# Kernel tuning notes

Hardware: AMD Instinct MI355X
Metric: run time of the kernel (lower is better)

The kernel has to match this reference:

```python
import jax, jax.numpy as jnp
import numpy as np

B, IN_SHAPE, EXP_SHAPE, HID, NB_CLASSES = 64, 10000, 53, 1500, 2048


def setup_inputs() -> dict:
    key = jax.random.key(0)
    ks = jax.random.split(key, 8)
    gos = jax.random.uniform(ks[0], (B, IN_SHAPE), dtype=jnp.float32)
    exp_x = jax.random.uniform(ks[1], (B, EXP_SHAPE), dtype=jnp.float32)
    # FlatModel params (torch Linear: y = x @ W.T + b; store pre-transposed)
    W1 = jax.random.normal(ks[2], (IN_SHAPE, HID), dtype=jnp.float32) * (1.0 / np.sqrt(IN_SHAPE))
    b1 = jnp.zeros((HID,), dtype=jnp.float32)
    W2 = jax.random.normal(ks[3], (HID + EXP_SHAPE, NB_CLASSES), dtype=jnp.float32) * (1.0 / np.sqrt(HID + EXP_SHAPE))
    b2 = jnp.zeros((NB_CLASSES,), dtype=jnp.float32)
    # HPO adjacency (non-trainable buffer in the original; values in [0,1))
    hpo_matrix = jax.random.uniform(ks[4], (NB_CLASSES, NB_CLASSES), dtype=jnp.float32)
    return {"gos": gos, "exp_x": exp_x, "W1": W1, "b1": b1, "W2": W2, "b2": b2, "hpo_matrix": hpo_matrix}


def reference(gos, exp_x, W1, b1, W2, b2, hpo_matrix):
    # FlatModel (eval mode: dropout is identity). torch F.gelu default = exact erf gelu.
    h = jax.nn.gelu(gos @ W1 + b1, approximate=False)          # (B, HID)
    x = jnp.concatenate([h, exp_x], axis=1)                     # (B, HID+EXP)
    flat = jax.nn.sigmoid(x @ W2 + b2)                          # (B, C)
    # HPOLayer + permute + MaxPool1d(C): out[b,j] = max_i flat[b,j] * M[i,j]
    out = jnp.max(flat[:, None, :] * hpo_matrix[None, :, :], axis=1)  # (B, C)
    return out
```

## Files before the change

### kernel.cpp

```cpp
#include <hip/hip_runtime.h>
#include <math.h>

#define B64 64
#define IN_SH 10000
#define EXP_SH 53
#define HID 1500
#define NPAD1 1536
#define NBC 2048
#define K2 1553
#define KS1 20
#define KST1 16
#define KS2 7
#define KST2 8
#define XSTEP 56
#define CMCH 32
#define CMBLK 256
#define WLDS 640

using short8  = __attribute__((ext_vector_type(8))) short;
using floatx4 = __attribute__((ext_vector_type(4))) float;
using uintx4  = __attribute__((ext_vector_type(4))) unsigned int;

__device__ __forceinline__ unsigned short f2bf(float f) {
    unsigned u = __float_as_uint(f);
    u += 0x7fffu + ((u >> 16) & 1u);
    return (unsigned short)(u >> 16);
}


__global__ __launch_bounds__(256) void prep_k(const float* __restrict__ g,
                                              unsigned short* __restrict__ gosBf,
                                              float* __restrict__ accz) {
    int bi = blockIdx.x;
    if (bi < 320) {
        int t    = bi * 256 + threadIdx.x;
        int lane = t & 63;
        int sgrp = (t >> 6) & 3;
        int step = t >> 8;
        int q    = lane >> 4;
        int l15  = lane & 15;
        int b    = sgrp * 16 + l15;
        int k0   = step * 32 + q * 8;
        const float* p = g + (size_t)b * IN_SH + k0;
        unsigned int o[4];
        #pragma unroll
        for (int i = 0; i < 4; i++) {
            float lo = (k0 + 2 * i     < IN_SH) ? p[2 * i]     : 0.f;
            float hi = (k0 + 2 * i + 1 < IN_SH) ? p[2 * i + 1] : 0.f;
            o[i] = (unsigned)f2bf(lo) | ((unsigned)f2bf(hi) << 16);
        }
        uintx4 v; v.x = o[0]; v.y = o[1]; v.z = o[2]; v.w = o[3];
        *(uintx4*)(gosBf + (size_t)t * 8) = v;
    } else {
        int t = (bi - 320) * 256 + threadIdx.x;
        floatx4 z = (floatx4){0.f, 0.f, 0.f, 0.f};
        #pragma unroll
        for (int i = 0; i < 28; i++)
            *(floatx4*)(accz + (size_t)(i * 2048 + t) * 4) = z;
    }
}

__device__ __forceinline__ void load_b4(const unsigned short* __restrict__ bf,
                                        int stg, uintx4 bv[4]) {
    #pragma unroll
    for (int s = 0; s < 4; s++)
        bv[s] = *(const uintx4*)(bf + (size_t)(stg * 4 + s) * 512);
}

template<int KSTEPS>
__device__ __forceinline__ void gemm_core(
    const float* __restrict__ W, const unsigned short* __restrict__ Bfc,
    float* __restrict__ accbuf, int N, int K, int ldw, int bx, int by, int tid,
    float* __restrict__ ldsw)
{
    int lane = tid & 63;
    int q    = lane >> 4;
    int l15  = lane & 15;
    int n0   = bx * 64 + 16 * (tid >> 6);
    int k0   = by * (KSTEPS * 32);
    bool fast = (n0 + 16 <= N) && (k0 + KSTEPS * 32 <= K);
    int kl  = lane >> 2;
    int c4  = (lane & 3) * 4;

    const unsigned short* bf = Bfc + (size_t)lane * 8;

    floatx4 acc[4];
    #pragma unroll
    for (int s = 0; s < 4; s++) acc[s] = (floatx4){0.f, 0.f, 0.f, 0.f};

    floatx4 g[2][2];

    #define GLB(st, slot)                                                        \
        {                                                                        \
            int kb_ = k0 + (st) * 32;                                            \
            _Pragma("unroll")                                                    \
            for (int i_ = 0; i_ < 2; i_++) {                                     \
                int kg_ = kb_ + kl + 16 * i_;                                    \
                if (fast) {                                                      \
                    g[slot][i_] = *(const floatx4*)(W + (size_t)kg_ * ldw + n0 + c4); \
                } else {                                                         \
                    _Pragma("unroll")                                            \
                    for (int j_ = 0; j_ < 4; j_++)                               \
                        g[slot][i_][j_] = (kg_ < K && n0 + c4 + j_ < N)          \
                            ? W[(size_t)kg_ * ldw + n0 + c4 + j_] : 0.f;         \
                }                                                                \
            }                                                                    \
        }
    #define LWR(buf, slot)                                                       \
        {                                                                        \
            _Pragma("unroll")                                                    \
            for (int i_ = 0; i_ < 2; i_++)                                       \
                *(floatx4*)(ldsw + (buf) * WLDS + (kl + 16 * i_) * 20 + c4) = g[slot][i_]; \
        }

    GLB(0, 0);
    if (KSTEPS > 1) GLB(1, 1);
    LWR(0, 0);

    uintx4 bv[2][4];
    load_b4(bf, 0, bv[0]);
    if (KSTEPS > 1) load_b4(bf, 1, bv[1]);

    #pragma unroll
    for (int st = 0; st < KSTEPS; st++) {
        const int s = st & 1;
        const float* lb = ldsw + s * WLDS;

        short8 af;
        #pragma unroll
        for (int j = 0; j < 8; j++)
            af[j] = (short)f2bf(lb[(q * 8 + j) * 20 + l15]);

        uintx4 bt[4];
        if (st + 2 < KSTEPS) {
            GLB(st + 2, s);
            load_b4(bf, st + 2, bt);
        }

        #pragma unroll
        for (int m = 0; m < 4; m++) {
            short8 bf8 = __builtin_bit_cast(short8, bv[s][m]);
            acc[m] = __builtin_amdgcn_mfma_f32_16x16x32_bf16(af, bf8, acc[m], 0, 0, 0);
        }

        if (st + 1 < KSTEPS) LWR(1 - s, 1 - s);
        if (st + 2 < KSTEPS) {
            #pragma unroll
            for (int m = 0; m < 4; m++) bv[s][m] = bt[m];
        }
    }
    #undef GLB
    #undef LWR

    int nrow = n0 + q * 4;
    #pragma unroll
    for (int s = 0; s < 4; s++) {
        #pragma unroll
        for (int rr = 0; rr < 4; rr++)
            atomicAdd(&accbuf[(size_t)(nrow + rr) * 64 + s * 16 + l15], acc[s][rr]);
    }
}

__global__ __launch_bounds__(256) void gemm1_k(
    const float* __restrict__ W1, const unsigned short* __restrict__ gosBf,
    float* __restrict__ hpre, const float* __restrict__ M, float* __restrict__ cm)
{
    __shared__ float lds[4 * 2 * WLDS];
    int bi = blockIdx.x;
    if (bi < CMBLK) {
        int j  = (bi & 7) * 256 + threadIdx.x;
        int i0 = (bi >> 3) * 64;
        float m = 0.0f;
        #pragma unroll 16
        for (int i = i0; i < i0 + 64; i++)
            m = fmaxf(m, M[(size_t)i * NBC + j]);
        cm[(bi >> 3) * NBC + j] = m;
    } else {
        int gb = bi - CMBLK;
        int bx = gb % 24;
        int by = gb / 24;
        gemm_core<KST1>(W1, gosBf + (size_t)by * (KST1 * 4) * 512,
                        hpre, HID, IN_SH, HID, bx, by,
                        threadIdx.x, lds + (threadIdx.x >> 6) * (2 * WLDS));
    }
}

__global__ __launch_bounds__(256) void gemm2_k(
    const float* __restrict__ W2, const unsigned short* __restrict__ Xf,
    float* __restrict__ logits)
{
    __shared__ float lds[4 * 2 * WLDS];
    gemm_core<KST2>(W2, Xf + (size_t)blockIdx.y * (KST2 * 4) * 512,
                    logits, NBC, K2, NBC, blockIdx.x, blockIdx.y,
                    threadIdx.x, lds + (threadIdx.x >> 6) * (2 * WLDS));
}

__global__ __launch_bounds__(256) void combine1(
    const float* __restrict__ hpre, const float* __restrict__ b1,
    const float* __restrict__ expx, unsigned short* __restrict__ Xf,
    const float* __restrict__ cm, float* __restrict__ cmr)
{
    int bi = blockIdx.x;
    if (bi < XSTEP) {
        int t    = bi * 256 + threadIdx.x;
        int lane = t & 63;
        int sgrp = (t >> 6) & 3;
        int step = t >> 8;
        int q    = lane >> 4;
        int l15  = lane & 15;
        int b    = sgrp * 16 + l15;
        int kb   = step * 32 + q * 8;
        unsigned int o[4];
        #pragma unroll
        for (int i = 0; i < 4; i++) {
            unsigned int lohi[2];
            #pragma unroll
            for (int h = 0; h < 2; h++) {
                int n = kb + 2 * i + h;
                float v = 0.f;
                if (n < HID) {
                    float s = hpre[(size_t)n * 64 + b] + b1[n];
                    v = 0.5f * s * (1.0f + erff(s * 0.70710678118654752f));
                } else if (n < HID + EXP_SH) {
                    v = expx[b * EXP_SH + (n - HID)];
                }
                lohi[h] = f2bf(v);
            }
            o[i] = lohi[0] | (lohi[1] << 16);
        }
        uintx4 v; v.x = o[0]; v.y = o[1]; v.z = o[2]; v.w = o[3];
        *(uintx4*)(Xf + (size_t)t * 8) = v;
    } else {
        int j = (bi - XSTEP) * 256 + threadIdx.x;
        float m = 0.f;
        #pragma unroll
        for (int c = 0; c < CMCH; c++) m = fmaxf(m, cm[c * NBC + j]);
        cmr[j] = m;
    }
}

__global__ __launch_bounds__(256) void final_k(
    const float* __restrict__ logits, const float* __restrict__ b2,
    const float* __restrict__ cmr, float* __restrict__ out)
{
    int idx = blockIdx.x * 256 + threadIdx.x;
    int b = idx & 63;
    int j = idx >> 6;
    float s = logits[(size_t)j * 64 + b] + b2[j];
    float sig = 1.0f / (1.0f + expf(-s));
    out[(size_t)b * NBC + j] = sig * cmr[j];
}

extern "C" void kernel_launch(void* const* d_in, const int* in_sizes, int n_in,
                              void* d_out, int out_size, void* d_ws, size_t ws_size,
                              hipStream_t stream) {
    const float* gos  = (const float*)d_in[0];
    const float* expx = (const float*)d_in[1];
    const float* W1   = (const float*)d_in[2];
    const float* b1   = (const float*)d_in[3];
    const float* W2   = (const float*)d_in[4];
    const float* b2   = (const float*)d_in[5];
    const float* hpo  = (const float*)d_in[6];
    float* out = (float*)d_out;

    char* ws = (char*)d_ws;
    unsigned short* gosBf = (unsigned short*)ws;
    float* hpre   = (float*)(ws + 1310720);
    float* logits = (float*)(ws + 1310720 + 393216);
    unsigned short* Xf = (unsigned short*)(ws + 2228224);
    float* cm  = (float*)(ws + 2228224 + 229376);
    float* cmr = (float*)(ws + 2228224 + 229376 + 262144);

    prep_k<<<328, 256, 0, stream>>>(gos, gosBf, hpre);

    gemm1_k<<<CMBLK + 24 * KS1, 256, 0, stream>>>(W1, gosBf, hpre, hpo, cm);

    combine1<<<XSTEP + 8, 256, 0, stream>>>(hpre, b1, expx, Xf, cm, cmr);

    gemm2_k<<<dim3(NBC / 64, KS2), 256, 0, stream>>>(W2, Xf, logits);

    final_k<<<(B64 * NBC) / 256, 256, 0, stream>>>(logits, b2, cmr, out);
}
```

Measured before the change: 154.0 us.

## Replace atomic split-K accumulation with per-slice partial buffers and doubled K splits

```diff
diff --git a/kernel.cpp b/kernel.cpp
--- a/kernel.cpp
+++ b/kernel.cpp
@@ -1,5 +1,6 @@
 #include <hip/hip_runtime.h>
 #include <math.h>
+
 
 #define B64 64
 #define IN_SH 10000
@@ -8,18 +9,21 @@
 #define NPAD1 1536
 #define NBC 2048
 #define K2 1553
-#define KS1 20
-#define KST1 16
-#define KS2 7
-#define KST2 8
+#define KS1 40
+#define KST1 8
+#define KS2 13
+#define KST2 4
 #define XSTEP 56
 #define CMCH 32
 #define CMBLK 256
 #define WLDS 640
+#define ACC1 (NPAD1 * 64)
+#define ACC2 (NBC * 64)
 
 using short8  = __attribute__((ext_vector_type(8))) short;
 using floatx4 = __attribute__((ext_vector_type(4))) float;
 using uintx4  = __attribute__((ext_vector_type(4))) unsigned int;
+using uintx2  = __attribute__((ext_vector_type(2))) unsigned int;
 
 __device__ __forceinline__ unsigned short f2bf(float f) {
     unsigned u = __float_as_uint(f);
@@ -29,35 +33,25 @@
 
 
 __global__ __launch_bounds__(256) void prep_k(const float* __restrict__ g,
-                                              unsigned short* __restrict__ gosBf,
-                                              float* __restrict__ accz) {
-    int bi = blockIdx.x;
-    if (bi < 320) {
-        int t    = bi * 256 + threadIdx.x;
-        int lane = t & 63;
-        int sgrp = (t >> 6) & 3;
-        int step = t >> 8;
-        int q    = lane >> 4;
-        int l15  = lane & 15;
-        int b    = sgrp * 16 + l15;
-        int k0   = step * 32 + q * 8;
-        const float* p = g + (size_t)b * IN_SH + k0;
-        unsigned int o[4];
-        #pragma unroll
-        for (int i = 0; i < 4; i++) {
-            float lo = (k0 + 2 * i     < IN_SH) ? p[2 * i]     : 0.f;
-            float hi = (k0 + 2 * i + 1 < IN_SH) ? p[2 * i + 1] : 0.f;
-            o[i] = (unsigned)f2bf(lo) | ((unsigned)f2bf(hi) << 16);
-        }
-        uintx4 v; v.x = o[0]; v.y = o[1]; v.z = o[2]; v.w = o[3];
-        *(uintx4*)(gosBf + (size_t)t * 8) = v;
-    } else {
-        int t = (bi - 320) * 256 + threadIdx.x;
-        floatx4 z = (floatx4){0.f, 0.f, 0.f, 0.f};
-        #pragma unroll
-        for (int i = 0; i < 28; i++)
-            *(floatx4*)(accz + (size_t)(i * 2048 + t) * 4) = z;
-    }
+                                              unsigned short* __restrict__ gosBf) {
+    int t    = blockIdx.x * 256 + threadIdx.x;
+    int lane = t & 63;
+    int sgrp = (t >> 6) & 3;
+    int step = t >> 8;
+    int q    = lane >> 4;
+    int l15  = lane & 15;
+    int b    = sgrp * 16 + l15;
+    int k0   = step * 32 + q * 8;
+    const float* p = g + (size_t)b * IN_SH + k0;
+    unsigned int o[4];
+    #pragma unroll
+    for (int i = 0; i < 4; i++) {
+        float lo = (k0 + 2 * i     < IN_SH) ? p[2 * i]     : 0.f;
+        float hi = (k0 + 2 * i + 1 < IN_SH) ? p[2 * i + 1] : 0.f;
+        o[i] = (unsigned)f2bf(lo) | ((unsigned)f2bf(hi) << 16);
+    }
+    uintx4 v; v.x = o[0]; v.y = o[1]; v.z = o[2]; v.w = o[3];
+    *(uintx4*)(gosBf + (size_t)t * 8) = v;
 }
 
 __device__ __forceinline__ void load_b4(const unsigned short* __restrict__ bf,
@@ -70,7 +64,7 @@
 template<int KSTEPS>
 __device__ __forceinline__ void gemm_core(
     const float* __restrict__ W, const unsigned short* __restrict__ Bfc,
-    float* __restrict__ accbuf, int N, int K, int ldw, int bx, int by, int tid,
+    float* __restrict__ pbuf, int N, int K, int ldw, int bx, int by, int tid,
     float* __restrict__ ldsw)
 {
     int lane = tid & 63;
@@ -157,13 +151,13 @@
     for (int s = 0; s < 4; s++) {
         #pragma unroll
         for (int rr = 0; rr < 4; rr++)
-            atomicAdd(&accbuf[(size_t)(nrow + rr) * 64 + s * 16 + l15], acc[s][rr]);
+            pbuf[(size_t)(nrow + rr) * 64 + s * 16 + l15] = acc[s][rr];
     }
 }
 
 __global__ __launch_bounds__(256) void gemm1_k(
     const float* __restrict__ W1, const unsigned short* __restrict__ gosBf,
-    float* __restrict__ hpre, const float* __restrict__ M, float* __restrict__ cm)
+    float* __restrict__ hpre_p, const float* __restrict__ M, float* __restrict__ cm)
 {
     __shared__ float lds[4 * 2 * WLDS];
     int bi = blockIdx.x;
@@ -180,58 +174,73 @@
         int bx = gb % 24;
         int by = gb / 24;
         gemm_core<KST1>(W1, gosBf + (size_t)by * (KST1 * 4) * 512,
-                        hpre, HID, IN_SH, HID, bx, by,
+                        hpre_p + (size_t)by * ACC1, HID, IN_SH, HID, bx, by,
                         threadIdx.x, lds + (threadIdx.x >> 6) * (2 * WLDS));
     }
 }
 
 __global__ __launch_bounds__(256) void gemm2_k(
     const float* __restrict__ W2, const unsigned short* __restrict__ Xf,
-    float* __restrict__ logits)
+    float* __restrict__ logits_p)
 {
     __shared__ float lds[4 * 2 * WLDS];
     gemm_core<KST2>(W2, Xf + (size_t)blockIdx.y * (KST2 * 4) * 512,
-                    logits, NBC, K2, NBC, blockIdx.x, blockIdx.y,
+                    logits_p + (size_t)blockIdx.y * ACC2, NBC, K2, NBC,
+                    blockIdx.x, blockIdx.y,
                     threadIdx.x, lds + (threadIdx.x >> 6) * (2 * WLDS));
 }
 
 __global__ __launch_bounds__(256) void combine1(
-    const float* __restrict__ hpre, const float* __restrict__ b1,
+    const float* __restrict__ hpre_p, const float* __restrict__ b1,
     const float* __restrict__ expx, unsigned short* __restrict__ Xf,
     const float* __restrict__ cm, float* __restrict__ cmr)
 {
     int bi = blockIdx.x;
-    if (bi < XSTEP) {
-        int t    = bi * 256 + threadIdx.x;
-        int lane = t & 63;
-        int sgrp = (t >> 6) & 3;
-        int step = t >> 8;
+    if (bi < 2 * XSTEP) {
+        int step = bi >> 1, half = bi & 1;
+        int tid  = threadIdx.x;
+        int lane = tid & 63;
+        int sgrp = tid >> 6;
         int q    = lane >> 4;
         int l15  = lane & 15;
         int b    = sgrp * 16 + l15;
         int kb   = step * 32 + q * 8;
-        unsigned int o[4];
-        #pragma unroll
-        for (int i = 0; i < 4; i++) {
-            unsigned int lohi[2];
+        int nb   = kb + half * 4;
+        float sv[4];
+        if (nb + 3 < HID) {
+            float s0 = b1[nb], s1 = b1[nb + 1], s2 = b1[nb + 2], s3 = b1[nb + 3];
+            const float* p = hpre_p + (size_t)nb * 64 + b;
+            #pragma unroll 8
+            for (int ks = 0; ks < KS1; ks++, p += ACC1) {
+                s0 += p[0]; s1 += p[64]; s2 += p[128]; s3 += p[192];
+            }
+            sv[0] = s0; sv[1] = s1; sv[2] = s2; sv[3] = s3;
             #pragma unroll
-            for (int h = 0; h < 2; h++) {
-                int n = kb + 2 * i + h;
+            for (int jj = 0; jj < 4; jj++)
+                sv[jj] = 0.5f * sv[jj] * (1.0f + erff(sv[jj] * 0.70710678118654752f));
+        } else {
+            #pragma unroll
+            for (int jj = 0; jj < 4; jj++) {
+                int n = nb + jj;
                 float v = 0.f;
                 if (n < HID) {
-                    float s = hpre[(size_t)n * 64 + b] + b1[n];
+                    float s = b1[n];
+                    for (int ks = 0; ks < KS1; ks++)
+                        s += hpre_p[(size_t)ks * ACC1 + (size_t)n * 64 + b];
                     v = 0.5f * s * (1.0f + erff(s * 0.70710678118654752f));
                 } else if (n < HID + EXP_SH) {
                     v = expx[b * EXP_SH + (n - HID)];
                 }
-                lohi[h] = f2bf(v);
+                sv[jj] = v;
             }
-            o[i] = lohi[0] | (lohi[1] << 16);
-        }
-        uintx4 v; v.x = o[0]; v.y = o[1]; v.z = o[2]; v.w = o[3];
-        *(uintx4*)(Xf + (size_t)t * 8) = v;
+        }
+        unsigned int o0 = (unsigned)f2bf(sv[0]) | ((unsigned)f2bf(sv[1]) << 16);
+        unsigned int o1 = (unsigned)f2bf(sv[2]) | ((unsigned)f2bf(sv[3]) << 16);
+        size_t t = (size_t)step * 256 + tid;
+        uintx2 v; v.x = o0; v.y = o1;
+        *(uintx2*)(Xf + t * 8 + half * 4) = v;
     } else {
-        int j = (bi - XSTEP) * 256 + threadIdx.x;
+        int j = (bi - 2 * XSTEP) * 256 + threadIdx.x;
         float m = 0.f;
         #pragma unroll
         for (int c = 0; c < CMCH; c++) m = fmaxf(m, cm[c * NBC + j]);
@@ -240,15 +249,34 @@
 }
 
 __global__ __launch_bounds__(256) void final_k(
-    const float* __restrict__ logits, const float* __restrict__ b2,
+    const float* __restrict__ logits_p, const float* __restrict__ b2,
     const float* __restrict__ cmr, float* __restrict__ out)
 {
-    int idx = blockIdx.x * 256 + threadIdx.x;
-    int b = idx & 63;
-    int j = idx >> 6;
-    float s = logits[(size_t)j * 64 + b] + b2[j];
-    float sig = 1.0f / (1.0f + expf(-s));
-    out[(size_t)b * NBC + j] = sig * cmr[j];
+    __shared__ float lds[32 * 65];
+    int j0  = blockIdx.x * 32;
+    int tid = threadIdx.x;
+    #pragma unroll
+    for (int e = 0; e < 8; e++) {
+        int lin = e * 256 + tid;
+        int jj  = lin >> 6;
+        int b   = lin & 63;
+        int j   = j0 + jj;
+        float s = b2[j];
+        const float* p = logits_p + (size_t)j * 64 + b;
+        #pragma unroll
+        for (int ks = 0; ks < KS2; ks++)
+            s += p[(size_t)ks * ACC2];
+        float sig = 1.0f / (1.0f + expf(-s));
+        lds[jj * 65 + b] = sig * cmr[j];
+    }
+    __syncthreads();
+    #pragma unroll
+    for (int e = 0; e < 8; e++) {
+        int lin = e * 256 + tid;
+        int b   = lin >> 5;
+        int jj  = lin & 31;
+        out[(size_t)b * NBC + j0 + jj] = lds[jj * 65 + b];
+    }
 }
 
 extern "C" void kernel_launch(void* const* d_in, const int* in_sizes, int n_in,
@@ -265,19 +293,19 @@
 
     char* ws = (char*)d_ws;
     unsigned short* gosBf = (unsigned short*)ws;
-    float* hpre   = (float*)(ws + 1310720);
-    float* logits = (float*)(ws + 1310720 + 393216);
-    unsigned short* Xf = (unsigned short*)(ws + 2228224);
-    float* cm  = (float*)(ws + 2228224 + 229376);
-    float* cmr = (float*)(ws + 2228224 + 229376 + 262144);
-
-    prep_k<<<328, 256, 0, stream>>>(gos, gosBf, hpre);
-
-    gemm1_k<<<CMBLK + 24 * KS1, 256, 0, stream>>>(W1, gosBf, hpre, hpo, cm);
-
-    combine1<<<XSTEP + 8, 256, 0, stream>>>(hpre, b1, expx, Xf, cm, cmr);
-
-    gemm2_k<<<dim3(NBC / 64, KS2), 256, 0, stream>>>(W2, Xf, logits);
-
-    final_k<<<(B64 * NBC) / 256, 256, 0, stream>>>(logits, b2, cmr, out);
-}
+    unsigned short* Xf    = (unsigned short*)(ws + 1310720);
+    float* cm       = (float*)(ws + 1540096);
+    float* cmr      = (float*)(ws + 1802240);
+    float* hpre_p   = (float*)(ws + 1810432);
+    float* logits_p = (float*)(ws + 17539072);
+
+    prep_k<<<320, 256, 0, stream>>>(gos, gosBf);
+
+    gemm1_k<<<CMBLK + 24 * KS1, 256, 0, stream>>>(W1, gosBf, hpre_p, hpo, cm);
+
+    combine1<<<2 * XSTEP + 8, 256, 0, stream>>>(hpre_p, b1, expx, Xf, cm, cmr);
+
+    gemm2_k<<<dim3(NBC / 64, KS2), 256, 0, stream>>>(W2, Xf, logits_p);
+
+    final_k<<<NBC / 32, 256, 0, stream>>>(logits_p, b2, cmr, out);
+}
```

Result: slower. 157.2 us (+2.1%).
